# Optimization experiments

Measured on AMD Instinct MI355X. Metric: run time of the kernel, lower is better.

Reference implementation:

```python
import jax, jax.numpy as jnp
import numpy as np

N = 50000      # n_nodes
E = 800000     # n_edges (avg degree 16)
IN, HID, CLS = 128, 128, 40


def setup_inputs() -> dict:
    key = jax.random.key(0)
    ks = jax.random.split(key, 9)
    features = jax.random.normal(ks[0], (N, IN), dtype=jnp.float32)
    src = jax.random.randint(ks[1], (E,), 0, N)
    dst = jax.random.randint(ks[2], (E,), 0, N)
    # GraphConv weights (glorot-ish scale) and biases
    W0 = jax.random.normal(ks[3], (IN, HID), dtype=jnp.float32) / np.sqrt(IN).astype(np.float32)
    b0 = jnp.zeros((HID,), jnp.float32)
    W1 = jax.random.normal(ks[4], (HID, HID), dtype=jnp.float32) / np.sqrt(HID).astype(np.float32)
    b1 = jnp.zeros((HID,), jnp.float32)
    W2 = jax.random.normal(ks[5], (HID, CLS), dtype=jnp.float32) / np.sqrt(HID).astype(np.float32)
    b2 = jnp.zeros((CLS,), jnp.float32)
    return {"features": features, "src": src, "dst": dst,
            "W0": W0, "b0": b0, "W1": W1, "b1": b1, "W2": W2, "b2": b2}


def _degree_norms(src, dst, dtype):
    # DGL GraphConv norm='both': D_out^{-1/2} on source side, D_in^{-1/2} on dest side,
    # degrees clamped to a minimum of 1.
    ones = jnp.ones(src.shape[0], dtype)
    deg_out = jax.ops.segment_sum(ones, src, num_segments=N)
    deg_in = jax.ops.segment_sum(ones, dst, num_segments=N)
    norm_out = jnp.where(deg_out > 0, deg_out, 1.0) ** -0.5
    norm_in = jnp.where(deg_in > 0, deg_in, 1.0) ** -0.5
    return norm_out, norm_in


def _graph_conv(h, src, dst, norm_out, norm_in, W, b, act):
    # h' = D_in^{-1/2} A D_out^{-1/2} h W + b ; optional relu
    h = (h * norm_out[:, None]) @ W            # dense transform first (in >= out)
    agg = jax.ops.segment_sum(h[src], dst, num_segments=N)  # sparse aggregation
    out = agg * norm_in[:, None] + b
    return jax.nn.relu(out) if act else out


def reference(features, src, dst, W0, b0, W1, b1, W2, b2):
    norm_out, norm_in = _degree_norms(src, dst, features.dtype)
    # dropout is identity in eval mode
    h = _graph_conv(features, src, dst, norm_out, norm_in, W0, b0, True)
    h = _graph_conv(h, src, dst, norm_out, norm_in, W1, b1, True)
    h = _graph_conv(h, src, dst, norm_out, norm_in, W2, b2, False)
    return h
```

## Files before the change

### kernel.cpp

```cpp
#include <hip/hip_runtime.h>
#include <hip/hip_fp16.h>


static constexpr int NN  = 50000;
static constexpr int NE  = 800000;
static constexpr int HID = 128;
static constexpr int CLS = 40;
static constexpr int CAP = 48;

static constexpr int NGEMM  = (NN + 127) / 128;
static constexpr int NBUILD = (NE + 255) / 256;

template <bool SCALE>
__device__ __forceinline__ void gemm128_body(const float* __restrict__ X,
                                             const float* __restrict__ W,
                                             const float* __restrict__ norm_out,
                                             __half* __restrict__ Y,
                                             int tileIdx, float* As, float* Bs) {
    constexpr int BSTR = 132;
    const int tid = threadIdx.x;
    const int rowBase = tileIdx * 128;

    const int bkk = tid >> 3;
    const int bc4 = tid & 7;
    const float* wrow = W + (size_t)bkk * 128 + bc4 * 16;

    const int rt = tid & 15;
    const int ct = tid >> 4;

    float acc[8][8];
    #pragma unroll
    for (int j = 0; j < 8; ++j)
        #pragma unroll
        for (int i = 0; i < 8; ++i) acc[j][i] = 0.f;

    float4 xv[4], wv[4];

    auto loadA = [&](int s) {
        #pragma unroll
        for (int i = 0; i < 4; ++i) {
            int f = tid + 256 * i;
            int r = f >> 3;
            int kc = f & 7;
            int grow = rowBase + r;
            xv[i] = (grow < NN)
                ? *(const float4*)(X + (size_t)grow * 128 + s * 32 + kc * 4)
                : make_float4(0.f, 0.f, 0.f, 0.f);
        }
    };
    auto loadB = [&](int s) {
        const float* p = wrow + (size_t)s * 32 * 128;
        #pragma unroll
        for (int i = 0; i < 4; ++i) wv[i] = ((const float4*)p)[i];
    };
    auto writeLDS = [&]() {
        #pragma unroll
        for (int i = 0; i < 4; ++i) {
            int f = tid + 256 * i;
            int r = f >> 3;
            int kc = f & 7;
            int pc = ((r >> 2) + kc) & 31;
            int base = pc * 4 + (r & 3);
            const float* v = (const float*)&xv[i];
            #pragma unroll
            for (int c = 0; c < 4; ++c)
                As[(kc * 4 + c) * 128 + base] = v[c];
        }
        #pragma unroll
        for (int i = 0; i < 4; ++i)
            *(float4*)&Bs[bkk * BSTR + bc4 * 16 + i * 4] = wv[i];
    };

    loadA(0); loadB(0);
    for (int s = 0; s < 4; ++s) {
        writeLDS();
        __syncthreads();
        if (s < 3) { loadA(s + 1); loadB(s + 1); }
        #pragma unroll 8
        for (int k = 0; k < 32; ++k) {
            int kc = k >> 2;
            int pa0 = (rt + kc) & 31;
            int pa1 = (rt + 16 + kc) & 31;
            float4 a0 = *(const float4*)&As[k * 128 + pa0 * 4];
            float4 a1 = *(const float4*)&As[k * 128 + pa1 * 4];
            float4 b0 = *(const float4*)&Bs[k * BSTR + ct * 8];
            float4 b1 = *(const float4*)&Bs[k * BSTR + ct * 8 + 4];
            float a[8] = {a0.x, a0.y, a0.z, a0.w, a1.x, a1.y, a1.z, a1.w};
            float b[8] = {b0.x, b0.y, b0.z, b0.w, b1.x, b1.y, b1.z, b1.w};
            #pragma unroll
            for (int j = 0; j < 8; ++j)
                #pragma unroll
                for (int ii = 0; ii < 8; ++ii)
                    acc[j][ii] = fmaf(a[j], b[ii], acc[j][ii]);
        }
        __syncthreads();
    }
    union Pack { __half2 h2[4]; uint4 u; };
    #pragma unroll
    for (int j = 0; j < 8; ++j) {
        int row = rowBase + ((j < 4) ? (4 * rt + j) : (64 + 4 * rt + (j - 4)));
        if (row < NN) {
            float nm = SCALE ? norm_out[row] : 1.f;
            Pack p;
            #pragma unroll
            for (int q = 0; q < 4; ++q)
                p.h2[q] = __halves2half2(__float2half_rn(acc[j][2 * q] * nm),
                                         __float2half_rn(acc[j][2 * q + 1] * nm));
            *(uint4*)(Y + (size_t)row * 128 + ct * 8) = p.u;
        }
    }
}

__global__ __launch_bounds__(256) void gemm128_kernel(const float* __restrict__ X,
                                                      const float* __restrict__ W,
                                                      const float* __restrict__ norm_out,
                                                      __half* __restrict__ Y) {
    __shared__ float As[32 * 128];
    __shared__ float Bs[32 * 132];
    gemm128_body<true>(X, W, norm_out, Y, blockIdx.x, As, Bs);
}

__global__ __launch_bounds__(256) void fused_kernel(const float* __restrict__ X,
                                                    const float* __restrict__ W0,
                                                    __half* __restrict__ Y,
                                                    const int* __restrict__ src,
                                                    const int* __restrict__ dst,
                                                    int* __restrict__ deg_out,
                                                    int* __restrict__ cnt,
                                                    unsigned short* __restrict__ colbkt) {
    __shared__ float As[32 * 128];
    __shared__ float Bs[32 * 132];
    int b = blockIdx.x;
    if (b < NGEMM) {
        gemm128_body<false>(X, W0, nullptr, Y, b, As, Bs);
    } else {
        int e = (b - NGEMM) * 256 + threadIdx.x;
        if (e < NE) {
            int s = src[e], d = dst[e];
            atomicAdd(&deg_out[s], 1);
            int slot = atomicAdd(&cnt[d], 1);
            if (slot < CAP) colbkt[(size_t)d * CAP + slot] = (unsigned short)s;
        }
    }
}

__global__ __launch_bounds__(256) void gemm40_kernel(const float* __restrict__ X,
                                                     const float* __restrict__ W,
                                                     const float* __restrict__ norm_out,
                                                     __half* __restrict__ Y) {
    __shared__ float As[32 * 128];
    __shared__ float Bs[32 * 40];
    const int tid = threadIdx.x;
    const int rowBase = blockIdx.x * 128;

    const int rt = tid & 31;
    const int ct = tid >> 5;

    float acc[4][5];
    #pragma unroll
    for (int j = 0; j < 4; ++j)
        #pragma unroll
        for (int c = 0; c < 5; ++c) acc[j][c] = 0.f;

    float4 xv[4], wv[2];

    auto loadA = [&](int s) {
        #pragma unroll
        for (int i = 0; i < 4; ++i) {
            int f = tid + 256 * i;
            int r = f >> 3;
            int kc = f & 7;
            int grow = rowBase + r;
            xv[i] = (grow < NN)
                ? *(const float4*)(X + (size_t)grow * 128 + s * 32 + kc * 4)
                : make_float4(0.f, 0.f, 0.f, 0.f);
        }
    };
    auto loadB = [&](int s) {
        #pragma unroll
        for (int i = 0; i < 2; ++i) {
            int f = tid + 256 * i;
            if (f < 320) {
                int kk = f / 10, c4 = f - kk * 10;
                wv[i] = *(const float4*)(W + (size_t)(s * 32 + kk) * 40 + c4 * 4);
            }
        }
    };
    auto writeLDS = [&]() {
        #pragma unroll
        for (int i = 0; i < 4; ++i) {
            int f = tid + 256 * i;
            int r = f >> 3;
            int kc = f & 7;
            int pc = ((r >> 2) + kc) & 31;
            int base = pc * 4 + (r & 3);
            const float* v = (const float*)&xv[i];
            #pragma unroll
            for (int c = 0; c < 4; ++c)
                As[(kc * 4 + c) * 128 + base] = v[c];
        }
        #pragma unroll
        for (int i = 0; i < 2; ++i) {
            int f = tid + 256 * i;
            if (f < 320) {
                int kk = f / 10, c4 = f - kk * 10;
                *(float4*)&Bs[kk * 40 + c4 * 4] = wv[i];
            }
        }
    };

    loadA(0); loadB(0);
    for (int s = 0; s < 4; ++s) {
        writeLDS();
        __syncthreads();
        if (s < 3) { loadA(s + 1); loadB(s + 1); }
        #pragma unroll 8
        for (int k = 0; k < 32; ++k) {
            int kc = k >> 2;
            int pa = (rt + kc) & 31;
            float4 a = *(const float4*)&As[k * 128 + pa * 4];
            float av[4] = {a.x, a.y, a.z, a.w};
            float bv[5];
            #pragma unroll
            for (int c = 0; c < 5; ++c) bv[c] = Bs[k * 40 + ct * 5 + c];
            #pragma unroll
            for (int j = 0; j < 4; ++j)
                #pragma unroll
                for (int c = 0; c < 5; ++c)
                    acc[j][c] = fmaf(av[j], bv[c], acc[j][c]);
        }
        __syncthreads();
    }
    #pragma unroll
    for (int j = 0; j < 4; ++j) {
        int row = rowBase + rt * 4 + j;
        if (row < NN) {
            float nm = norm_out[row];
            #pragma unroll
            for (int c = 0; c < 5; ++c)
                Y[(size_t)row * 40 + ct * 5 + c] = __float2half_rn(acc[j][c] * nm);
        }
    }
}

__global__ __launch_bounds__(256) void norm_kernel(const int* __restrict__ deg_out,
                                                   const int* __restrict__ cnt,
                                                   float* __restrict__ norm_out,
                                                   float* __restrict__ norm_in) {
    int v = blockIdx.x * 256 + threadIdx.x;
    if (v < NN) {
        int dof = deg_out[v], dif = cnt[v];
        norm_out[v] = rsqrtf((float)(dof > 0 ? dof : 1));
        norm_in[v]  = rsqrtf((float)(dif > 0 ? dif : 1));
    }
}

template <bool WEIGHTED, bool RELU>
__global__ __launch_bounds__(256) void agg128h_kernel(const __half* __restrict__ T,
                                                      const unsigned short* __restrict__ colbkt,
                                                      const int* __restrict__ cnt,
                                                      const float* __restrict__ norm_out,
                                                      const float* __restrict__ norm_in,
                                                      const float* __restrict__ bias,
                                                      float* __restrict__ out) {
    int node = blockIdx.x * 4 + (threadIdx.x >> 6);
    int lane = threadIdx.x & 63;
    if (node >= NN) return;
    int dg = cnt[node];
    if (dg > CAP) dg = CAP;
    const unsigned short* bkt = colbkt + (size_t)node * CAP;
    const int grp = lane >> 4;
    const int l16 = lane & 15;

    float acc[8];
    #pragma unroll
    for (int i = 0; i < 8; ++i) acc[i] = 0.f;

    constexpr int B = 4;
    for (int j = 0; j < dg; j += 4 * B) {
        uint4 v[B];
        float w[B];
        #pragma unroll
        for (int u = 0; u < B; ++u) {
            int e  = j + 4 * u + grp;
            int ec = e < dg ? e : dg - 1;
            int s  = (int)bkt[ec];
            w[u]   = e < dg ? (WEIGHTED ? norm_out[s] : 1.f) : 0.f;
            v[u]   = ((const uint4*)(T + (size_t)s * 128))[l16];
        }
        #pragma unroll
        for (int u = 0; u < B; ++u) {
            const __half2* hp = (const __half2*)&v[u];
            #pragma unroll
            for (int q = 0; q < 4; ++q) {
                float2 f = __half22float2(hp[q]);
                acc[2 * q]     = fmaf(f.x, w[u], acc[2 * q]);
                acc[2 * q + 1] = fmaf(f.y, w[u], acc[2 * q + 1]);
            }
        }
    }
    #pragma unroll
    for (int i = 0; i < 8; ++i) {
        acc[i] += __shfl_xor(acc[i], 16, 64);
        acc[i] += __shfl_xor(acc[i], 32, 64);
    }
    if (grp == 0) {
        float nm = norm_in[node];
        float4 b0 = ((const float4*)bias)[l16 * 2];
        float4 b1 = ((const float4*)bias)[l16 * 2 + 1];
        float4 o0, o1;
        o0.x = fmaf(acc[0], nm, b0.x); o0.y = fmaf(acc[1], nm, b0.y);
        o0.z = fmaf(acc[2], nm, b0.z); o0.w = fmaf(acc[3], nm, b0.w);
        o1.x = fmaf(acc[4], nm, b1.x); o1.y = fmaf(acc[5], nm, b1.y);
        o1.z = fmaf(acc[6], nm, b1.z); o1.w = fmaf(acc[7], nm, b1.w);
        if (RELU) {
            o0.x = fmaxf(o0.x, 0.f); o0.y = fmaxf(o0.y, 0.f);
            o0.z = fmaxf(o0.z, 0.f); o0.w = fmaxf(o0.w, 0.f);
            o1.x = fmaxf(o1.x, 0.f); o1.y = fmaxf(o1.y, 0.f);
            o1.z = fmaxf(o1.z, 0.f); o1.w = fmaxf(o1.w, 0.f);
        }
        ((float4*)(out + (size_t)node * 128))[l16 * 2]     = o0;
        ((float4*)(out + (size_t)node * 128))[l16 * 2 + 1] = o1;
    }
}

__global__ __launch_bounds__(256) void agg40h_kernel(const __half* __restrict__ T,
                                                     const unsigned short* __restrict__ colbkt,
                                                     const int* __restrict__ cnt,
                                                     const float* __restrict__ norm_in,
                                                     const float* __restrict__ bias,
                                                     float* __restrict__ out) {
    int node = blockIdx.x * 4 + (threadIdx.x >> 6);
    int lane = threadIdx.x & 63;
    if (node >= NN) return;
    int dg = cnt[node];
    if (dg > CAP) dg = CAP;
    const unsigned short* bkt = colbkt + (size_t)node * CAP;
    const int grp = lane / 20;
    const int l20 = lane - grp * 20;

    float accx = 0.f, accy = 0.f;
    constexpr int B = 4;
    for (int j = 0; j < dg; j += 3 * B) {
        unsigned int v[B];
        float w[B];
        #pragma unroll
        for (int u = 0; u < B; ++u) {
            int e  = j + 3 * u + grp;
            bool p = (grp < 3) && (e < dg);
            int ec = e < dg ? e : dg - 1;
            int s  = (grp < 3) ? (int)bkt[ec] : 0;
            w[u]   = p ? 1.f : 0.f;
            v[u]   = *(const unsigned int*)(T + (size_t)s * 40 + l20 * 2);
        }
        #pragma unroll
        for (int u = 0; u < B; ++u) {
            float2 f = __half22float2(*(const __half2*)&v[u]);
            accx = fmaf(f.x, w[u], accx);
            accy = fmaf(f.y, w[u], accy);
        }
    }
    accx += __shfl(accx, lane + 20, 64) + __shfl(accx, lane + 40, 64);
    accy += __shfl(accy, lane + 20, 64) + __shfl(accy, lane + 40, 64);

    if (lane < 20) {
        float nm = norm_in[node];
        float2 b = *(const float2*)(bias + lane * 2);
        float ox = fmaf(accx, nm, b.x);
        float oy = fmaf(accy, nm, b.y);
        *(float2*)(out + (size_t)node * 40 + lane * 2) = make_float2(ox, oy);
    }
}

extern "C" void kernel_launch(void* const* d_in, const int* in_sizes, int n_in,
                              void* d_out, int out_size, void* d_ws, size_t ws_size,
                              hipStream_t stream) {
    const float* features = (const float*)d_in[0];
    const int*   src      = (const int*)d_in[1];
    const int*   dst      = (const int*)d_in[2];
    const float* W0       = (const float*)d_in[3];
    const float* b0       = (const float*)d_in[4];
    const float* W1       = (const float*)d_in[5];
    const float* b1       = (const float*)d_in[6];
    const float* W2       = (const float*)d_in[7];
    const float* b2       = (const float*)d_in[8];
    float*       out      = (float*)d_out;

    char* ws = (char*)d_ws;
    auto alloc = [&](size_t bytes) {
        char* p = ws;
        ws += (bytes + 511) & ~(size_t)511;
        return p;
    };
    int*            deg_out  = (int*)alloc((size_t)NN * 4);
    int*            cnt      = (int*)alloc((size_t)NN * 4);
    float*          norm_out = (float*)alloc((size_t)NN * 4);
    float*          norm_in  = (float*)alloc((size_t)NN * 4);
    unsigned short* colbkt   = (unsigned short*)alloc((size_t)NN * CAP * 2);
    __half*         t        = (__half*)alloc((size_t)NN * HID * 2);
    float*          h        = (float*)alloc((size_t)NN * HID * 4);
    if ((size_t)(ws - (char*)d_ws) > ws_size) return;

    hipMemsetAsync(deg_out, 0, (size_t)NN * 4, stream);
    hipMemsetAsync(cnt, 0, (size_t)NN * 4, stream);

    int gAgg = (NN + 3) / 4;

    fused_kernel<<<NGEMM + NBUILD, 256, 0, stream>>>(features, W0, t, src, dst,
                                                     deg_out, cnt, colbkt);
    norm_kernel<<<(NN + 255) / 256, 256, 0, stream>>>(deg_out, cnt, norm_out, norm_in);

    agg128h_kernel<true, true><<<gAgg, 256, 0, stream>>>(t, colbkt, cnt, norm_out, norm_in, b0, h);
    gemm128_kernel<<<NGEMM, 256, 0, stream>>>(h, W1, norm_out, t);
    agg128h_kernel<false, true><<<gAgg, 256, 0, stream>>>(t, colbkt, cnt, norm_out, norm_in, b1, h);
    gemm40_kernel<<<NGEMM, 256, 0, stream>>>(h, W2, norm_out, t);
    agg40h_kernel<<<gAgg, 256, 0, stream>>>(t, colbkt, cnt, norm_in, b2, out);
}
```

Before: 320.4 us.

## Store hidden activations in fp16, use MFMA for layer-1 GEMM, prescale features

Intermediate activations h are now stored as fp16 rather than fp32, which halves the traffic of the aggregation writes and the GEMM reads. The layer-1 dense transform runs on MFMA 16x16x32 f16 instructions, with W1 transposed and converted to fp16 inside the fused build kernel. The source-degree scaling of layer 0 moves out of the per-edge gather into a norm_scale pass that rescales t in place, so the aggregation no longer gathers norm_out per edge. The cost is extra rounding to fp16, one more pass over t, and uncoalesced 2-byte stores in the MFMA epilogue.

```diff
diff --git a/kernel.cpp b/kernel.cpp
--- a/kernel.cpp
+++ b/kernel.cpp
@@ -10,11 +10,13 @@
 
 static constexpr int NGEMM  = (NN + 127) / 128;
 static constexpr int NBUILD = (NE + 255) / 256;
-
-template <bool SCALE>
+static constexpr int NPREP  = 8;
+
+typedef __attribute__((ext_vector_type(8))) _Float16 f16x8;
+typedef __attribute__((ext_vector_type(4))) float    f32x4;
+
 __device__ __forceinline__ void gemm128_body(const float* __restrict__ X,
                                              const float* __restrict__ W,
-                                             const float* __restrict__ norm_out,
                                              __half* __restrict__ Y,
                                              int tileIdx, float* As, float* Bs) {
     constexpr int BSTR = 132;
@@ -100,24 +102,14 @@
     for (int j = 0; j < 8; ++j) {
         int row = rowBase + ((j < 4) ? (4 * rt + j) : (64 + 4 * rt + (j - 4)));
         if (row < NN) {
-            float nm = SCALE ? norm_out[row] : 1.f;
             Pack p;
             #pragma unroll
             for (int q = 0; q < 4; ++q)
-                p.h2[q] = __halves2half2(__float2half_rn(acc[j][2 * q] * nm),
-                                         __float2half_rn(acc[j][2 * q + 1] * nm));
+                p.h2[q] = __halves2half2(__float2half_rn(acc[j][2 * q]),
+                                         __float2half_rn(acc[j][2 * q + 1]));
             *(uint4*)(Y + (size_t)row * 128 + ct * 8) = p.u;
         }
     }
-}
-
-__global__ __launch_bounds__(256) void gemm128_kernel(const float* __restrict__ X,
-                                                      const float* __restrict__ W,
-                                                      const float* __restrict__ norm_out,
-                                                      __half* __restrict__ Y) {
-    __shared__ float As[32 * 128];
-    __shared__ float Bs[32 * 132];
-    gemm128_body<true>(X, W, norm_out, Y, blockIdx.x, As, Bs);
 }
 
 __global__ __launch_bounds__(256) void fused_kernel(const float* __restrict__ X,
@@ -127,13 +119,15 @@
                                                     const int* __restrict__ dst,
                                                     int* __restrict__ deg_out,
                                                     int* __restrict__ cnt,
-                                                    unsigned short* __restrict__ colbkt) {
+                                                    unsigned short* __restrict__ colbkt,
+                                                    const float* __restrict__ W1,
+                                                    __half* __restrict__ W1t) {
     __shared__ float As[32 * 128];
     __shared__ float Bs[32 * 132];
     int b = blockIdx.x;
     if (b < NGEMM) {
-        gemm128_body<false>(X, W0, nullptr, Y, b, As, Bs);
-    } else {
+        gemm128_body(X, W0, Y, b, As, Bs);
+    } else if (b < NGEMM + NBUILD) {
         int e = (b - NGEMM) * 256 + threadIdx.x;
         if (e < NE) {
             int s = src[e], d = dst[e];
@@ -141,10 +135,79 @@
             int slot = atomicAdd(&cnt[d], 1);
             if (slot < CAP) colbkt[(size_t)d * CAP + slot] = (unsigned short)s;
         }
-    }
-}
-
-__global__ __launch_bounds__(256) void gemm40_kernel(const float* __restrict__ X,
+    } else {
+        int gid = (b - NGEMM - NBUILD) * 256 + threadIdx.x;
+        int n = gid >> 4, q = gid & 15;
+        union { __half h[8]; uint4 u; } p;
+        #pragma unroll
+        for (int j = 0; j < 8; ++j)
+            p.h[j] = __float2half_rn(W1[(size_t)(q * 8 + j) * 128 + n]);
+        ((uint4*)W1t)[n * 16 + ((q + n) & 15)] = p.u;
+    }
+}
+
+__global__ __launch_bounds__(256) void gemm1_mfma(const __half* __restrict__ H,
+                                                  const __half* __restrict__ W1t,
+                                                  const float* __restrict__ norm_out,
+                                                  __half* __restrict__ T) {
+    __shared__ __half Ws[128 * 128];
+    const int tid = threadIdx.x;
+    #pragma unroll
+    for (int i = 0; i < 8; ++i)
+        ((uint4*)Ws)[tid + 256 * i] = ((const uint4*)W1t)[tid + 256 * i];
+
+    const int wv   = tid >> 6;
+    const int lane = tid & 63;
+    const int m    = lane & 15;
+    const int quad = lane >> 4;
+    const int rowW = blockIdx.x * 64 + wv * 16;
+
+    union AB { uint4 u; f16x8 h; };
+    AB a[4];
+    int arow = rowW + m;
+    if (arow >= NN) arow = NN - 1;
+    const uint4* hp = (const uint4*)(H + (size_t)arow * 128);
+    #pragma unroll
+    for (int kc = 0; kc < 4; ++kc)
+        a[kc].u = hp[kc * 4 + quad];
+
+    __syncthreads();
+
+    f32x4 acc[8];
+    #pragma unroll
+    for (int nt = 0; nt < 8; ++nt) acc[nt] = (f32x4){0.f, 0.f, 0.f, 0.f};
+
+    #pragma unroll
+    for (int kc = 0; kc < 4; ++kc) {
+        #pragma unroll
+        for (int nt = 0; nt < 8; ++nt) {
+            int n = nt * 16 + m;
+            int q = kc * 4 + quad;
+            AB bf;
+            bf.u = ((const uint4*)Ws)[n * 16 + ((q + n) & 15)];
+            acc[nt] = __builtin_amdgcn_mfma_f32_16x16x32_f16(a[kc].h, bf.h, acc[nt], 0, 0, 0);
+        }
+    }
+
+    float nmv[4];
+    #pragma unroll
+    for (int r = 0; r < 4; ++r) {
+        int row = rowW + quad * 4 + r;
+        nmv[r] = (row < NN) ? norm_out[row] : 0.f;
+    }
+    #pragma unroll
+    for (int nt = 0; nt < 8; ++nt) {
+        int coln = nt * 16 + m;
+        #pragma unroll
+        for (int r = 0; r < 4; ++r) {
+            int row = rowW + quad * 4 + r;
+            if (row < NN)
+                T[(size_t)row * 128 + coln] = __float2half_rn(acc[nt][r] * nmv[r]);
+        }
+    }
+}
+
+__global__ __launch_bounds__(256) void gemm40_kernel(const __half* __restrict__ X,
                                                      const float* __restrict__ W,
                                                      const float* __restrict__ norm_out,
                                                      __half* __restrict__ Y) {
@@ -162,18 +225,19 @@
         #pragma unroll
         for (int c = 0; c < 5; ++c) acc[j][c] = 0.f;
 
-    float4 xv[4], wv[2];
+    uint4 xu[2];
+    float4 wv[2];
 
     auto loadA = [&](int s) {
         #pragma unroll
-        for (int i = 0; i < 4; ++i) {
+        for (int i = 0; i < 2; ++i) {
             int f = tid + 256 * i;
-            int r = f >> 3;
-            int kc = f & 7;
+            int r = f >> 2;
+            int c = f & 3;
             int grow = rowBase + r;
-            xv[i] = (grow < NN)
-                ? *(const float4*)(X + (size_t)grow * 128 + s * 32 + kc * 4)
-                : make_float4(0.f, 0.f, 0.f, 0.f);
+            xu[i] = (grow < NN)
+                ? *(const uint4*)(X + (size_t)grow * 128 + s * 32 + c * 8)
+                : make_uint4(0, 0, 0, 0);
         }
     };
     auto loadB = [&](int s) {
@@ -188,16 +252,19 @@
     };
     auto writeLDS = [&]() {
         #pragma unroll
-        for (int i = 0; i < 4; ++i) {
+        for (int i = 0; i < 2; ++i) {
             int f = tid + 256 * i;
-            int r = f >> 3;
-            int kc = f & 7;
-            int pc = ((r >> 2) + kc) & 31;
-            int base = pc * 4 + (r & 3);
-            const float* v = (const float*)&xv[i];
-            #pragma unroll
-            for (int c = 0; c < 4; ++c)
-                As[(kc * 4 + c) * 128 + base] = v[c];
+            int r = f >> 2;
+            int c = f & 3;
+            const __half2* hp = (const __half2*)&xu[i];
+            #pragma unroll
+            for (int q = 0; q < 4; ++q) {
+                float2 f2 = __half22float2(hp[q]);
+                int k0 = c * 8 + 2 * q;
+                int pc = ((r >> 2) + (k0 >> 2)) & 31;
+                As[k0 * 128 + pc * 4 + (r & 3)]       = f2.x;
+                As[(k0 + 1) * 128 + pc * 4 + (r & 3)] = f2.y;
+            }
         }
         #pragma unroll
         for (int i = 0; i < 2; ++i) {
@@ -218,8 +285,8 @@
         for (int k = 0; k < 32; ++k) {
             int kc = k >> 2;
             int pa = (rt + kc) & 31;
-            float4 a = *(const float4*)&As[k * 128 + pa * 4];
-            float av[4] = {a.x, a.y, a.z, a.w};
+            float4 av4 = *(const float4*)&As[k * 128 + pa * 4];
+            float av[4] = {av4.x, av4.y, av4.z, av4.w};
             float bv[5];
             #pragma unroll
             for (int c = 0; c < 5; ++c) bv[c] = Bs[k * 40 + ct * 5 + c];
@@ -243,26 +310,51 @@
     }
 }
 
-__global__ __launch_bounds__(256) void norm_kernel(const int* __restrict__ deg_out,
-                                                   const int* __restrict__ cnt,
-                                                   float* __restrict__ norm_out,
-                                                   float* __restrict__ norm_in) {
-    int v = blockIdx.x * 256 + threadIdx.x;
-    if (v < NN) {
-        int dof = deg_out[v], dif = cnt[v];
-        norm_out[v] = rsqrtf((float)(dof > 0 ? dof : 1));
-        norm_in[v]  = rsqrtf((float)(dif > 0 ? dif : 1));
-    }
-}
-
-template <bool WEIGHTED, bool RELU>
+__global__ __launch_bounds__(256) void norm_scale_kernel(const int* __restrict__ deg_out,
+                                                         const int* __restrict__ cnt,
+                                                         float* __restrict__ norm_out,
+                                                         float* __restrict__ norm_in,
+                                                         __half* __restrict__ t) {
+    __shared__ float nms[32];
+    int base = blockIdx.x * 32;
+    int tid = threadIdx.x;
+    if (tid < 32) {
+        int v = base + tid;
+        float no = 1.f;
+        if (v < NN) {
+            int dof = deg_out[v], dif = cnt[v];
+            no = rsqrtf((float)(dof > 0 ? dof : 1));
+            norm_out[v] = no;
+            norm_in[v]  = rsqrtf((float)(dif > 0 ? dif : 1));
+        }
+        nms[tid] = no;
+    }
+    __syncthreads();
+    for (int i = tid; i < 512; i += 256) {
+        int ro = i >> 4, ch = i & 15;
+        int v = base + ro;
+        if (v < NN) {
+            uint4* p = (uint4*)t + (size_t)v * 16 + ch;
+            uint4 u = *p;
+            float nm = nms[ro];
+            __half2* hp = (__half2*)&u;
+            #pragma unroll
+            for (int q = 0; q < 4; ++q) {
+                float2 f = __half22float2(hp[q]);
+                hp[q] = __halves2half2(__float2half_rn(f.x * nm),
+                                       __float2half_rn(f.y * nm));
+            }
+            *p = u;
+        }
+    }
+}
+
 __global__ __launch_bounds__(256) void agg128h_kernel(const __half* __restrict__ T,
                                                       const unsigned short* __restrict__ colbkt,
                                                       const int* __restrict__ cnt,
-                                                      const float* __restrict__ norm_out,
                                                       const float* __restrict__ norm_in,
                                                       const float* __restrict__ bias,
-                                                      float* __restrict__ out) {
+                                                      __half* __restrict__ out) {
     int node = blockIdx.x * 4 + (threadIdx.x >> 6);
     int lane = threadIdx.x & 63;
     if (node >= NN) return;
@@ -285,7 +377,7 @@
             int e  = j + 4 * u + grp;
             int ec = e < dg ? e : dg - 1;
             int s  = (int)bkt[ec];
-            w[u]   = e < dg ? (WEIGHTED ? norm_out[s] : 1.f) : 0.f;
+            w[u]   = e < dg ? 1.f : 0.f;
             v[u]   = ((const uint4*)(T + (size_t)s * 128))[l16];
         }
         #pragma unroll
@@ -308,19 +400,19 @@
         float nm = norm_in[node];
         float4 b0 = ((const float4*)bias)[l16 * 2];
         float4 b1 = ((const float4*)bias)[l16 * 2 + 1];
-        float4 o0, o1;
-        o0.x = fmaf(acc[0], nm, b0.x); o0.y = fmaf(acc[1], nm, b0.y);
-        o0.z = fmaf(acc[2], nm, b0.z); o0.w = fmaf(acc[3], nm, b0.w);
-        o1.x = fmaf(acc[4], nm, b1.x); o1.y = fmaf(acc[5], nm, b1.y);
-        o1.z = fmaf(acc[6], nm, b1.z); o1.w = fmaf(acc[7], nm, b1.w);
-        if (RELU) {
-            o0.x = fmaxf(o0.x, 0.f); o0.y = fmaxf(o0.y, 0.f);
-            o0.z = fmaxf(o0.z, 0.f); o0.w = fmaxf(o0.w, 0.f);
-            o1.x = fmaxf(o1.x, 0.f); o1.y = fmaxf(o1.y, 0.f);
-            o1.z = fmaxf(o1.z, 0.f); o1.w = fmaxf(o1.w, 0.f);
-        }
-        ((float4*)(out + (size_t)node * 128))[l16 * 2]     = o0;
-        ((float4*)(out + (size_t)node * 128))[l16 * 2 + 1] = o1;
+        float o[8];
+        o[0] = fmaf(acc[0], nm, b0.x); o[1] = fmaf(acc[1], nm, b0.y);
+        o[2] = fmaf(acc[2], nm, b0.z); o[3] = fmaf(acc[3], nm, b0.w);
+        o[4] = fmaf(acc[4], nm, b1.x); o[5] = fmaf(acc[5], nm, b1.y);
+        o[6] = fmaf(acc[6], nm, b1.z); o[7] = fmaf(acc[7], nm, b1.w);
+        union { __half2 h2[4]; uint4 u; } pk;
+        #pragma unroll
+        for (int q = 0; q < 4; ++q) {
+            float x = fmaxf(o[2 * q], 0.f);
+            float y = fmaxf(o[2 * q + 1], 0.f);
+            pk.h2[q] = __halves2half2(__float2half_rn(x), __float2half_rn(y));
+        }
+        ((uint4*)(out + (size_t)node * 128))[l16] = pk.u;
     }
 }
 
@@ -397,8 +489,9 @@
     float*          norm_out = (float*)alloc((size_t)NN * 4);
     float*          norm_in  = (float*)alloc((size_t)NN * 4);
     unsigned short* colbkt   = (unsigned short*)alloc((size_t)NN * CAP * 2);
+    __half*         W1t      = (__half*)alloc((size_t)HID * HID * 2);
     __half*         t        = (__half*)alloc((size_t)NN * HID * 2);
-    float*          h        = (float*)alloc((size_t)NN * HID * 4);
+    __half*         h        = (__half*)alloc((size_t)NN * HID * 2);
     if ((size_t)(ws - (char*)d_ws) > ws_size) return;
 
     hipMemsetAsync(deg_out, 0, (size_t)NN * 4, stream);
@@ -406,13 +499,13 @@
 
     int gAgg = (NN + 3) / 4;
 
-    fused_kernel<<<NGEMM + NBUILD, 256, 0, stream>>>(features, W0, t, src, dst,
-                                                     deg_out, cnt, colbkt);
-    norm_kernel<<<(NN + 255) / 256, 256, 0, stream>>>(deg_out, cnt, norm_out, norm_in);
-
-    agg128h_kernel<true, true><<<gAgg, 256, 0, stream>>>(t, colbkt, cnt, norm_out, norm_in, b0, h);
-    gemm128_kernel<<<NGEMM, 256, 0, stream>>>(h, W1, norm_out, t);
-    agg128h_kernel<false, true><<<gAgg, 256, 0, stream>>>(t, colbkt, cnt, norm_out, norm_in, b1, h);
+    fused_kernel<<<NGEMM + NBUILD + NPREP, 256, 0, stream>>>(
+        features, W0, t, src, dst, deg_out, cnt, colbkt, W1, W1t);
+    norm_scale_kernel<<<(NN + 31) / 32, 256, 0, stream>>>(deg_out, cnt, norm_out, norm_in, t);
+
+    agg128h_kernel<<<gAgg, 256, 0, stream>>>(t, colbkt, cnt, norm_in, b0, h);
+    gemm1_mfma<<<(NN + 63) / 64, 256, 0, stream>>>(h, W1t, norm_out, t);
+    agg128h_kernel<<<gAgg, 256, 0, stream>>>(t, colbkt, cnt, norm_in, b1, h);
     gemm40_kernel<<<NGEMM, 256, 0, stream>>>(h, W2, norm_out, t);
     agg40h_kernel<<<gAgg, 256, 0, stream>>>(t, colbkt, cnt, norm_in, b2, out);
 }
```

Result: faster. 294.3 us (-8.1%).
